# Kernel tuning notes

Hardware: AMD Instinct MI355X
Metric: run time of the kernel (lower is better)

The kernel has to match this reference:

```python
import jax, jax.numpy as jnp
from jax import lax
import numpy as np

B, S, D, COMP = 4, 1024, 512, 4


def setup_inputs() -> dict:
    key = jax.random.key(0)
    x = jax.random.normal(key, (B * S, D), dtype=jnp.float32)
    return {"x": x, "comp_rate": COMP, "seqlen": S}


def _merge_step(x, t, seq):
    # x: [seq, D], compacted so the k = seq - t valid tokens occupy rows 0..k-1.
    xn = jnp.roll(x, -1, axis=0)  # x[i+1] (wrap value never selected among valid pairs)
    # dist only feeds argmax (non-differentiable), mirror torch exactly; stop_gradient
    # keeps the vjp from saving residuals for this dead-for-gradients path.
    xg = lax.stop_gradient(x)
    dist = jnp.sum(xg * jnp.roll(xg, -1, axis=0), axis=-1)  # scalar_product metric
    j = jnp.arange(x.shape[0])
    dist = jnp.where(j < seq - 1 - t, dist, -jnp.inf)  # k-1 valid adjacent pairs
    mid = jnp.argmax(dist)
    jm = j[:, None]
    # rows < mid keep, row mid becomes (x[mid]+x[mid+1])/2, rows > mid shift left by 1
    return jnp.where(jm < mid, x, jnp.where(jm == mid, (x + xn) * 0.5, xn))


def _merge_sample(x, steps, seq):
    def body(carry, t):
        return _merge_step(carry, t, seq), None
    x, _ = lax.scan(body, x, jnp.arange(steps))
    return x


def reference(x, comp_rate, seqlen):
    d = x.shape[-1]
    b = x.shape[0] // seqlen
    n_comp = seqlen // comp_rate
    steps = seqlen - n_comp
    xb = x.reshape(b, seqlen, d)
    merged = jax.vmap(lambda xs: _merge_sample(xs, steps, seqlen))(xb)
    # torch smart_merge concatenates per-sample results along dim 0
    return merged[:, :n_comp].reshape(b * n_comp, d)
```

## Files before the change

### kernel.cpp

```cpp
#include <hip/hip_runtime.h>
#include <math.h>

#define S 1024
#define D 512
#define NCOMP (S / 4)
#define STEPS (S - NCOMP)
#define NEG_INF (-__builtin_inff())

__device__ int g_iter = 0;

__device__ __forceinline__ int   f2i(float x) { return __builtin_bit_cast(int, x); }
__device__ __forceinline__ float i2f(int x)   { return __builtin_bit_cast(float, x); }
__device__ __forceinline__ int   rfl(int x)   { return __builtin_amdgcn_readfirstlane(x); }

__device__ __forceinline__ unsigned fkey(float f) {
    unsigned u = __builtin_bit_cast(unsigned, f);
    return (u & 0x80000000u) ? ~u : (u | 0x80000000u);
}
__device__ __forceinline__ float unfkey(unsigned k) {
    unsigned u = (k & 0x80000000u) ? (k & 0x7fffffffu) : ~k;
    return __builtin_bit_cast(float, u);
}

__device__ __forceinline__ float wave_sum63(float x) {
    x += i2f(__builtin_amdgcn_update_dpp(0, f2i(x), 0x111, 0xF, 0xF, true));
    x += i2f(__builtin_amdgcn_update_dpp(0, f2i(x), 0x112, 0xF, 0xF, true));
    x += i2f(__builtin_amdgcn_update_dpp(0, f2i(x), 0x114, 0xF, 0xF, true));
    x += i2f(__builtin_amdgcn_update_dpp(0, f2i(x), 0x118, 0xF, 0xF, true));
    x += i2f(__builtin_amdgcn_update_dpp(0, f2i(x), 0x142, 0xA, 0xF, true));
    x += i2f(__builtin_amdgcn_update_dpp(0, f2i(x), 0x143, 0xC, 0xF, true));
    return x;
}

#define AMAX_STEP(ctrl, rm) do {                                                        \
    unsigned ok_ = (unsigned)__builtin_amdgcn_update_dpp((int)key, (int)key, (ctrl), (rm), 0xF, false); \
    int      oi_ = __builtin_amdgcn_update_dpp(bi, bi, (ctrl), (rm), 0xF, false);        \
    bool tk_ = (ok_ > key) || ((ok_ == key) && (oi_ < bi));                              \
    key = tk_ ? ok_ : key; bi = tk_ ? oi_ : bi;                                          \
} while (0)

struct Row { float4 a, b; };

__device__ __forceinline__ Row row_load(const float* vals, int slot, int lane) {
    const float4* p = (const float4*)(vals + (size_t)slot * D);
    Row r; r.a = p[lane * 2]; r.b = p[lane * 2 + 1]; return r;
}
__device__ __forceinline__ void row_store(float* vals, int slot, int lane, Row r) {
    float4* p = (float4*)(vals + (size_t)slot * D);
    p[lane * 2] = r.a; p[lane * 2 + 1] = r.b;
}
__device__ __forceinline__ Row row_avg(Row x, Row y) {
    Row r;
    r.a.x = (x.a.x + y.a.x) * 0.5f; r.a.y = (x.a.y + y.a.y) * 0.5f;
    r.a.z = (x.a.z + y.a.z) * 0.5f; r.a.w = (x.a.w + y.a.w) * 0.5f;
    r.b.x = (x.b.x + y.b.x) * 0.5f; r.b.y = (x.b.y + y.b.y) * 0.5f;
    r.b.z = (x.b.z + y.b.z) * 0.5f; r.b.w = (x.b.w + y.b.w) * 0.5f;
    return r;
}
__device__ __forceinline__ float dot8_partial(Row x, Row y) {
    float acc = x.a.x * y.a.x;
    acc += x.a.y * y.a.y; acc += x.a.z * y.a.z; acc += x.a.w * y.a.w;
    acc += x.b.x * y.b.x; acc += x.b.y * y.b.y; acc += x.b.z * y.b.z; acc += x.b.w * y.b.w;
    return acc;
}
__device__ __forceinline__ int lsr(int s) { return ((unsigned)s < (unsigned)S) ? s : 0; }
__device__ __forceinline__ int lsl(int s) { return ((unsigned)s <= (unsigned)S) ? s : 0; }

__device__ __forceinline__ void lds_argmax(const float* dist, int lane, float& v1, int& i1) {
    float av[16];
#pragma unroll
    for (int k = 0; k < 16; ++k) av[k] = dist[lane + 64 * k];
    float v8[8]; int k8[8];
#pragma unroll
    for (int k = 0; k < 8; ++k) { bool tk = av[k+8] > av[k]; v8[k] = tk ? av[k+8] : av[k]; k8[k] = tk ? (k+8) : k; }
    float v4[4]; int k4[4];
#pragma unroll
    for (int k = 0; k < 4; ++k) { bool tk = v8[k+4] > v8[k]; v4[k] = tk ? v8[k+4] : v8[k]; k4[k] = tk ? k8[k+4] : k8[k]; }
    float v2[2]; int k2[2];
#pragma unroll
    for (int k = 0; k < 2; ++k) { bool tk = v4[k+2] > v4[k]; v2[k] = tk ? v4[k+2] : v4[k]; k2[k] = tk ? k4[k+2] : k4[k]; }
    bool tk1 = v2[1] > v2[0];
    float lv = tk1 ? v2[1] : v2[0];
    int   lk = tk1 ? k2[1] : k2[0];
    unsigned key = fkey(lv);
    int bi = lane | (lk << 6);
    AMAX_STEP(0x111, 0xF); AMAX_STEP(0x112, 0xF);
    AMAX_STEP(0x114, 0xF); AMAX_STEP(0x118, 0xF);
    AMAX_STEP(0x142, 0xA); AMAX_STEP(0x143, 0xC);
    i1 = __builtin_amdgcn_readlane(bi, 63);
    v1 = unfkey((unsigned)__builtin_amdgcn_readlane((int)key, 63));
}

__device__ __attribute__((noinline)) void merge_A(float* __restrict__ vb,
                                                  const float* __restrict__ sd,
                                                  int* __restrict__ outIdx, int lane) {
    __shared__ int4 linksA[S + 1];
    __shared__ float distA[S];
    int4* links = linksA; float* dist = distA;

    for (int s = lane; s <= S; s += 64)
        links[s] = (s >= S) ? make_int4(S, S, S, 0)
                            : make_int4(s - 1, s + 1, (s + 2 <= S) ? (s + 2) : S, 0);
#pragma unroll
    for (int k = 0; k < 16; ++k) dist[lane + 64 * k] = sd[lane + 64 * k];

    float v1; int i1;
    lds_argmax(dist, lane, v1, i1);
    int m = i1;
    int4 L0 = links[m];
    int p = rfl(L0.x);
    int r = rfl(L0.y);
    int q = rfl(L0.z);
    bool hasp = (p >= 0), hasq = (q < S);
    int pp = hasp ? rfl(links[lsl(p)].x) : -1;
    int nq = hasq ? rfl(links[lsl(q)].y) : S;
    Row Rp  = row_load(vb, lsr(p),  lane);
    Row Rm  = row_load(vb, m,       lane);
    Row Rr  = row_load(vb, r,       lane);
    Row Rq  = row_load(vb, lsr(q),  lane);
    Row Rpp = row_load(vb, lsr(pp), lane);
    Row Rnq = row_load(vb, lsr(nq), lane);

#pragma unroll 1
    for (int t = 0; t < STEPS; ++t) {
        if (lane == 0) {
            links[m].y = q; links[m].z = nq;
            if (hasp) links[p].z = q;
            if (hasq) links[q].x = m;
            dist[m] = NEG_INF; dist[r] = NEG_INF;
            if (hasp) dist[p] = NEG_INF;
        }
        Row vm = row_avg(Rm, Rr);
        row_store(vb, m, lane, vm);
        if (t + 1 >= STEPS) break;

        float sp_ = wave_sum63(dot8_partial(Rp, vm));
        float sq_ = wave_sum63(dot8_partial(vm, Rq));
        float ndp = hasp ? i2f(__builtin_amdgcn_readlane(f2i(sp_), 63)) : NEG_INF;
        float ndm = hasq ? i2f(__builtin_amdgcn_readlane(f2i(sq_), 63)) : NEG_INF;

        lds_argmax(dist, lane, v1, i1);

        float best = v1; int bi = i1;
        if (hasp && (ndp > best || (ndp == best && p < bi))) { best = ndp; bi = p; }
        if (hasq && (ndm > best || (ndm == best && m < bi))) { best = ndm; bi = m; }
        const int m2 = bi;

        if (lane == 0) {
            if (hasp) dist[p] = ndp;
            if (hasq) dist[m] = ndm;
        }

        int4 Li = links[lsl(i1)];
        int p2 = rfl(Li.x);
        int r2 = rfl(Li.y);
        int q2 = rfl(Li.z);
        int4 Lp2 = links[lsl(p2)];
        int4 Lq2 = links[lsl(q2)];
        int pp2 = (p2 >= 0) ? rfl(Lp2.x) : -1;
        int nq2 = (q2 < S)  ? rfl(Lq2.y) : S;
        Row Sp  = (p2 == m)  ? vm : row_load(vb, lsr(p2),  lane);
        Row Si  = row_load(vb, lsr(i1), lane);
        Row Sr  = row_load(vb, lsr(r2), lane);
        Row Sq  = (q2 == m)  ? vm : row_load(vb, lsr(q2),  lane);
        Row Spp = (pp2 == m) ? vm : row_load(vb, lsr(pp2), lane);
        Row Snq = (nq2 == m) ? vm : row_load(vb, lsr(nq2), lane);

        if (m2 == m) {
            int nnq = S;
            if (nq < S) nnq = rfl(links[nq].y);
            Row Rnq2 = (nnq < S) ? row_load(vb, lsr(nnq), lane) : Rnq;
            Rm = vm; Rr = Rq; Rq = Rnq; Rnq = Rnq2;
            r = q; q = nq; nq = nnq;
            hasq = (q < S);
        } else if (m2 == p) {
            int npp = -1;
            if (pp >= 0) npp = rfl(links[pp].x);
            Row Rpp2 = (npp >= 0) ? row_load(vb, lsr(npp), lane) : Rpp;
            Rr = vm; Rm = Rp; Rp = Rpp; Rpp = Rpp2;
            r = m; m = p; p = pp; pp = npp;
            hasp = (p >= 0);
        } else {
            m = i1; p = p2; r = r2; q = q2; pp = pp2; nq = nq2;
            Rm = Si; Rr = Sr; Rp = Sp; Rq = Sq; Rpp = Spp; Rnq = Snq;
            hasp = (p >= 0); hasq = (q < S);
        }
    }

    if (lane == 0) {
        int s = 0;
        for (int i = 0; i < NCOMP; i += 2) {
            outIdx[i] = s;
            int4 Ls = links[s];
            if (i + 1 < NCOMP) outIdx[i + 1] = Ls.y;
            s = Ls.z;
        }
    }
}

__device__ __attribute__((noinline)) void merge_B(float* __restrict__ vb,
                                                  const float* __restrict__ sd,
                                                  int* __restrict__ outIdx, int lane) {
    __shared__ int4 linksB[S + 1];
    __shared__ float distB[S];
    int4* links = linksB; float* dist = distB;
    const int* li32 = (const int*)linksB;

    for (int s = lane; s <= S; s += 64)
        links[s] = (s >= S) ? make_int4(S, S, S, 0)
                            : make_int4(s - 1, s + 1, (s + 2 <= S) ? (s + 2) : S, 0);
#pragma unroll
    for (int k = 0; k < 16; ++k) dist[lane + 64 * k] = sd[lane + 64 * k];

    float v1; int i1;
    lds_argmax(dist, lane, v1, i1);
    int m = i1;
    int4 L0 = links[m];
    int p = rfl(L0.x);
    int r = rfl(L0.y);
    int q = rfl(L0.z);
    bool hasp = (p >= 0), hasq = (q < S);
    int pp = hasp ? rfl(links[lsl(p)].x) : -1;
    int nq = hasq ? rfl(links[lsl(q)].y) : S;
    Row Rp  = row_load(vb, lsr(p),  lane);
    Row Rm  = row_load(vb, m,       lane);
    Row Rr  = row_load(vb, r,       lane);
    Row Rq  = row_load(vb, lsr(q),  lane);
    bool pendP = false, pendQ = false;
    Row vmprev = Rm;

#pragma unroll 1
    for (int t = 0; t < STEPS; ++t) {
        Row RppL = row_load(vb, lsr(pp), lane);
        Row RnqL = row_load(vb, lsr(nq), lane);
        int wnnq = li32[lsl(nq) * 4 + 1];
        int wnpp = li32[lsl(pp) * 4 + 0];

        if (lane == 0) {
            links[m].y = q; links[m].z = nq;
            if (hasp) links[p].z = q;
            if (hasq) links[q].x = m;
            dist[m] = NEG_INF; dist[r] = NEG_INF;
            if (hasp) dist[p] = NEG_INF;
        }
        Row vm = row_avg(Rm, Rr);
        row_store(vb, m, lane, vm);
        if (t + 1 >= STEPS) break;

        float sp_ = wave_sum63(dot8_partial(Rp, vm));
        float sq_ = wave_sum63(dot8_partial(vm, Rq));
        float ndp = hasp ? i2f(__builtin_amdgcn_readlane(f2i(sp_), 63)) : NEG_INF;
        float ndm = hasq ? i2f(__builtin_amdgcn_readlane(f2i(sq_), 63)) : NEG_INF;

        lds_argmax(dist, lane, v1, i1);

        float best = v1; int bi = i1;
        if (hasp && (ndp > best || (ndp == best && p < bi))) { best = ndp; bi = p; }
        if (hasq && (ndm > best || (ndm == best && m < bi))) { best = ndm; bi = m; }
        const int m2 = bi;

        if (lane == 0) {
            if (hasp) dist[p] = ndp;
            if (hasq) dist[m] = ndm;
        }

        int4 Li = links[lsl(i1)];
        int p2 = rfl(Li.x);
        int r2 = rfl(Li.y);
        int q2 = rfl(Li.z);
        int pp2 = rfl(li32[lsl(p2) * 4 + 0]);
        int nq2 = rfl(li32[lsl(q2) * 4 + 1]);
        Row Si = row_load(vb, lsr(i1), lane);
        Row Sr = row_load(vb, lsr(r2), lane);
        Row Sp = (p2 == m) ? vm : row_load(vb, lsr(p2), lane);
        Row Sq = (q2 == m) ? vm : row_load(vb, lsr(q2), lane);

        Row Rpp_eff = pendP ? vmprev : RppL;
        Row Rnq_eff = pendQ ? vmprev : RnqL;

        if (m2 == m) {
            Rm = vm; Rr = Rq; Rq = Rnq_eff;
            r = q; q = nq; nq = rfl(wnnq);
            hasq = (q < S);
            pendP = false; pendQ = false;
        } else if (m2 == p) {
            Rr = vm; Rm = Rp; Rp = Rpp_eff;
            r = m; m = p; p = pp; pp = rfl(wnpp);
            hasp = (p >= 0);
            pendP = false; pendQ = false;
        } else {
            pendP = (pp2 == m); pendQ = (nq2 == m); vmprev = vm;
            m = i1; p = p2; r = r2; q = q2; pp = pp2; nq = nq2;
            Rm = Si; Rr = Sr; Rp = Sp; Rq = Sq;
            hasp = (p >= 0); hasq = (q < S);
        }
    }

    if (lane == 0) {
        int s = 0;
        for (int i = 0; i < NCOMP; i += 2) {
            outIdx[i] = s;
            int4 Ls = links[s];
            if (i + 1 < NCOMP) outIdx[i + 1] = Ls.y;
            s = Ls.z;
        }
    }
}

__global__ __launch_bounds__(256) void init_kernel(const float* __restrict__ x,
                                                   float* __restrict__ vals,
                                                   float* __restrict__ out) {
    const int blk = blockIdx.x, b = blk >> 4, g = blk & 15;
    const int tid = threadIdx.x, lane = tid & 63, w = tid >> 6;
    const float* xb = x + (size_t)b * S * D;
    if (blk == 0 && tid == 0) g_iter = g_iter + 1;
    if (vals != x) {
        float* vb = vals + (size_t)b * S * D;
        const float4* s4 = (const float4*)xb;
        float4* d4 = (float4*)vb;
        const int base = g * (S * D / 4 / 16);
        for (int i = tid; i < S * D / 4 / 16; i += 256) d4[base + i] = s4[base + i];
    }
    float* sd = out + (size_t)b * NCOMP * D;
#pragma unroll 1
    for (int j = 0; j < 16; ++j) {
        int pr = g * 64 + w * 16 + j;
        if (pr < S - 1) {
            Row A = row_load(xb, pr, lane);
            Row B = row_load(xb, pr + 1, lane);
            float t = wave_sum63(dot8_partial(A, B));
            if (lane == 63) sd[pr] = t;
        }
    }
    if (g == 0 && tid == 0) sd[S - 1] = NEG_INF;
}

__global__ __launch_bounds__(256, 1) void merge_kernel(float* __restrict__ vals,
                                                       float* __restrict__ out,
                                                       int nb) {
    const int blk = blockIdx.x, tid = threadIdx.x;
    const int b = blk, lane = tid & 63, wave = tid >> 6;
    float* vb = vals + (size_t)b * S * D;
    float* aux = out + (size_t)b * NCOMP * D;
    const float* sd = aux;
    int* outIdx = (int*)(aux + S);

    if (wave != 0) {
        float acc = 0.0f;
        for (int s = wave - 1; s < S; s += 3) {
            Row rr = row_load(vb, s, lane);
            acc += rr.a.x + rr.b.w;
        }
        if (acc == 1234.5678f) out[2050] = acc;
        return;
    }

    if (g_iter & 1) merge_A(vb, sd, outIdx, lane);
    else            merge_B(vb, sd, outIdx, lane);
}

__global__ __launch_bounds__(256) void gather_kernel(const float* __restrict__ vals,
                                                     float* __restrict__ out) {
    const int b = blockIdx.x, part = blockIdx.y;
    const float* vb = vals + (size_t)b * S * D;
    float* ob = out + (size_t)b * NCOMP * D;
    __shared__ int oi[NCOMP / 8];
    const int row0 = part * (NCOMP / 8);
    if (threadIdx.x < NCOMP / 8)
        oi[threadIdx.x] = ((const int*)(ob + S))[row0 + threadIdx.x];
    __syncthreads();
    const float4* v4 = (const float4*)vb;
    float4* o4 = (float4*)ob;
    const int per = (NCOMP / 8) * (D / 4);
    for (int idx = threadIdx.x; idx < per; idx += 256) {
        int row = idx >> 7, c = idx & 127;
        o4[(size_t)(row0 + row) * (D / 4) + c] = v4[(size_t)oi[row] * (D / 4) + c];
    }
}

extern "C" void kernel_launch(void* const* d_in, const int* in_sizes, int n_in,
                              void* d_out, int out_size, void* d_ws, size_t ws_size,
                              hipStream_t stream) {
    const float* x = (const float*)d_in[0];
    float* out = (float*)d_out;
    const int b = in_sizes[0] / (S * D);
    const size_t need = (size_t)in_sizes[0] * sizeof(float);
    float* vals = (ws_size >= need) ? (float*)d_ws : (float*)x;
    init_kernel<<<dim3(16 * b), dim3(256), 0, stream>>>(x, vals, out);
    merge_kernel<<<dim3(b), dim3(256), 0, stream>>>(vals, out, b);
    gather_kernel<<<dim3(b, 8), dim3(256), 0, stream>>>(vals, out);
}
```

Before: 1.041 ms.

## Offload per-step LDS argmax to a second wave via LDS mailbox handshake

Adds a merge_dual path in which wave 1 computes the argmax over the dist array while wave 0 does the row averaging, dot products and link updates for the same step. The two waves hand off through a small shared-memory mailbox using acquire/release atomics and spin-waits. Neighbour row and link loads are also issued earlier in the step. The aim is to take the argmax reduction off the serial critical path of each merge step. The cost is spin-wait overhead, and only calls with even g_iter use the new path, because the kernel still alternates it with the old single-wave version.

```diff
diff --git a/kernel.cpp b/kernel.cpp
--- a/kernel.cpp
+++ b/kernel.cpp
@@ -66,7 +66,8 @@
 __device__ __forceinline__ int lsr(int s) { return ((unsigned)s < (unsigned)S) ? s : 0; }
 __device__ __forceinline__ int lsl(int s) { return ((unsigned)s <= (unsigned)S) ? s : 0; }
 
-__device__ __forceinline__ void lds_argmax(const float* dist, int lane, float& v1, int& i1) {
+__device__ __forceinline__ void lds_argmax_raw(const float* dist, int lane,
+                                               unsigned& key_out, int& bi_out) {
     float av[16];
 #pragma unroll
     for (int k = 0; k < 16; ++k) av[k] = dist[lane + 64 * k];
@@ -87,120 +88,16 @@
     AMAX_STEP(0x111, 0xF); AMAX_STEP(0x112, 0xF);
     AMAX_STEP(0x114, 0xF); AMAX_STEP(0x118, 0xF);
     AMAX_STEP(0x142, 0xA); AMAX_STEP(0x143, 0xC);
-    i1 = __builtin_amdgcn_readlane(bi, 63);
-    v1 = unfkey((unsigned)__builtin_amdgcn_readlane((int)key, 63));
-}
-
-__device__ __attribute__((noinline)) void merge_A(float* __restrict__ vb,
-                                                  const float* __restrict__ sd,
-                                                  int* __restrict__ outIdx, int lane) {
-    __shared__ int4 linksA[S + 1];
-    __shared__ float distA[S];
-    int4* links = linksA; float* dist = distA;
-
-    for (int s = lane; s <= S; s += 64)
-        links[s] = (s >= S) ? make_int4(S, S, S, 0)
-                            : make_int4(s - 1, s + 1, (s + 2 <= S) ? (s + 2) : S, 0);
-#pragma unroll
-    for (int k = 0; k < 16; ++k) dist[lane + 64 * k] = sd[lane + 64 * k];
-
-    float v1; int i1;
-    lds_argmax(dist, lane, v1, i1);
-    int m = i1;
-    int4 L0 = links[m];
-    int p = rfl(L0.x);
-    int r = rfl(L0.y);
-    int q = rfl(L0.z);
-    bool hasp = (p >= 0), hasq = (q < S);
-    int pp = hasp ? rfl(links[lsl(p)].x) : -1;
-    int nq = hasq ? rfl(links[lsl(q)].y) : S;
-    Row Rp  = row_load(vb, lsr(p),  lane);
-    Row Rm  = row_load(vb, m,       lane);
-    Row Rr  = row_load(vb, r,       lane);
-    Row Rq  = row_load(vb, lsr(q),  lane);
-    Row Rpp = row_load(vb, lsr(pp), lane);
-    Row Rnq = row_load(vb, lsr(nq), lane);
-
-#pragma unroll 1
-    for (int t = 0; t < STEPS; ++t) {
-        if (lane == 0) {
-            links[m].y = q; links[m].z = nq;
-            if (hasp) links[p].z = q;
-            if (hasq) links[q].x = m;
-            dist[m] = NEG_INF; dist[r] = NEG_INF;
-            if (hasp) dist[p] = NEG_INF;
-        }
-        Row vm = row_avg(Rm, Rr);
-        row_store(vb, m, lane, vm);
-        if (t + 1 >= STEPS) break;
-
-        float sp_ = wave_sum63(dot8_partial(Rp, vm));
-        float sq_ = wave_sum63(dot8_partial(vm, Rq));
-        float ndp = hasp ? i2f(__builtin_amdgcn_readlane(f2i(sp_), 63)) : NEG_INF;
-        float ndm = hasq ? i2f(__builtin_amdgcn_readlane(f2i(sq_), 63)) : NEG_INF;
-
-        lds_argmax(dist, lane, v1, i1);
-
-        float best = v1; int bi = i1;
-        if (hasp && (ndp > best || (ndp == best && p < bi))) { best = ndp; bi = p; }
-        if (hasq && (ndm > best || (ndm == best && m < bi))) { best = ndm; bi = m; }
-        const int m2 = bi;
-
-        if (lane == 0) {
-            if (hasp) dist[p] = ndp;
-            if (hasq) dist[m] = ndm;
-        }
-
-        int4 Li = links[lsl(i1)];
-        int p2 = rfl(Li.x);
-        int r2 = rfl(Li.y);
-        int q2 = rfl(Li.z);
-        int4 Lp2 = links[lsl(p2)];
-        int4 Lq2 = links[lsl(q2)];
-        int pp2 = (p2 >= 0) ? rfl(Lp2.x) : -1;
-        int nq2 = (q2 < S)  ? rfl(Lq2.y) : S;
-        Row Sp  = (p2 == m)  ? vm : row_load(vb, lsr(p2),  lane);
-        Row Si  = row_load(vb, lsr(i1), lane);
-        Row Sr  = row_load(vb, lsr(r2), lane);
-        Row Sq  = (q2 == m)  ? vm : row_load(vb, lsr(q2),  lane);
-        Row Spp = (pp2 == m) ? vm : row_load(vb, lsr(pp2), lane);
-        Row Snq = (nq2 == m) ? vm : row_load(vb, lsr(nq2), lane);
-
-        if (m2 == m) {
-            int nnq = S;
-            if (nq < S) nnq = rfl(links[nq].y);
-            Row Rnq2 = (nnq < S) ? row_load(vb, lsr(nnq), lane) : Rnq;
-            Rm = vm; Rr = Rq; Rq = Rnq; Rnq = Rnq2;
-            r = q; q = nq; nq = nnq;
-            hasq = (q < S);
-        } else if (m2 == p) {
-            int npp = -1;
-            if (pp >= 0) npp = rfl(links[pp].x);
-            Row Rpp2 = (npp >= 0) ? row_load(vb, lsr(npp), lane) : Rpp;
-            Rr = vm; Rm = Rp; Rp = Rpp; Rpp = Rpp2;
-            r = m; m = p; p = pp; pp = npp;
-            hasp = (p >= 0);
-        } else {
-            m = i1; p = p2; r = r2; q = q2; pp = pp2; nq = nq2;
-            Rm = Si; Rr = Sr; Rp = Sp; Rq = Sq; Rpp = Spp; Rnq = Snq;
-            hasp = (p >= 0); hasq = (q < S);
-        }
-    }
-
-    if (lane == 0) {
-        int s = 0;
-        for (int i = 0; i < NCOMP; i += 2) {
-            outIdx[i] = s;
-            int4 Ls = links[s];
-            if (i + 1 < NCOMP) outIdx[i + 1] = Ls.y;
-            s = Ls.z;
-        }
-    }
-}
-
-__device__ __attribute__((noinline)) void merge_B(float* __restrict__ vb,
-                                                  const float* __restrict__ sd,
-                                                  int* __restrict__ outIdx, int lane) {
+    bi_out  = __builtin_amdgcn_readlane(bi, 63);
+    key_out = (unsigned)__builtin_amdgcn_readlane((int)key, 63);
+}
+__device__ __forceinline__ void lds_argmax(const float* dist, int lane, float& v1, int& i1) {
+    unsigned key; lds_argmax_raw(dist, lane, key, i1); v1 = unfkey(key);
+}
+
+__device__ __attribute__((noinline)) void merge_single(float* __restrict__ vb,
+                                                       const float* __restrict__ sd,
+                                                       int* __restrict__ outIdx, int lane) {
     __shared__ int4 linksB[S + 1];
     __shared__ float distB[S];
     int4* links = linksB; float* dist = distB;
@@ -307,6 +204,145 @@
     }
 }
 
+__device__ __attribute__((noinline)) void merge_dual(float* __restrict__ vb,
+                                                     const float* __restrict__ sd,
+                                                     int* __restrict__ outIdx,
+                                                     int lane, int wave,
+                                                     int* __restrict__ mbox) {
+    __shared__ int4 linksD[S + 1];
+    __shared__ float distD[S];
+    int4* links = linksD; float* dist = distD;
+    const int* li32 = (const int*)linksD;
+
+    if (wave == 1) {
+#pragma unroll 1
+        for (int t = 0; t < STEPS - 1; ++t) {
+            while (__hip_atomic_load(&mbox[0], __ATOMIC_ACQUIRE,
+                                     __HIP_MEMORY_SCOPE_WORKGROUP) < t + 1) {}
+            unsigned key; int bi;
+            lds_argmax_raw(dist, lane, key, bi);
+            if (lane == 0) {
+                mbox[2] = (int)key; mbox[3] = bi;
+                __hip_atomic_store(&mbox[1], t + 1, __ATOMIC_RELEASE,
+                                   __HIP_MEMORY_SCOPE_WORKGROUP);
+            }
+        }
+        return;
+    }
+
+    for (int s = lane; s <= S; s += 64)
+        links[s] = (s >= S) ? make_int4(S, S, S, 0)
+                            : make_int4(s - 1, s + 1, (s + 2 <= S) ? (s + 2) : S, 0);
+#pragma unroll
+    for (int k = 0; k < 16; ++k) dist[lane + 64 * k] = sd[lane + 64 * k];
+
+    float v1; int i1;
+    lds_argmax(dist, lane, v1, i1);
+    int m = i1;
+    int4 L0 = links[m];
+    int p = rfl(L0.x);
+    int r = rfl(L0.y);
+    int q = rfl(L0.z);
+    bool hasp = (p >= 0), hasq = (q < S);
+    int pp = hasp ? rfl(links[lsl(p)].x) : -1;
+    int nq = hasq ? rfl(links[lsl(q)].y) : S;
+    Row Rp  = row_load(vb, lsr(p),  lane);
+    Row Rm  = row_load(vb, m,       lane);
+    Row Rr  = row_load(vb, r,       lane);
+    Row Rq  = row_load(vb, lsr(q),  lane);
+    bool pendP = false, pendQ = false;
+    Row vmprev = Rm;
+
+#pragma unroll 1
+    for (int t = 0; t < STEPS - 1; ++t) {
+        Row RppL = row_load(vb, lsr(pp), lane);
+        Row RnqL = row_load(vb, lsr(nq), lane);
+        int wnnq = li32[lsl(nq) * 4 + 1];
+        int wnpp = li32[lsl(pp) * 4 + 0];
+
+        if (lane == 0) {
+            links[m].y = q; links[m].z = nq;
+            if (hasp) links[p].z = q;
+            if (hasq) links[q].x = m;
+            dist[m] = NEG_INF; dist[r] = NEG_INF;
+            if (hasp) dist[p] = NEG_INF;
+            __hip_atomic_store(&mbox[0], t + 1, __ATOMIC_RELEASE,
+                               __HIP_MEMORY_SCOPE_WORKGROUP);
+        }
+
+        Row vm = row_avg(Rm, Rr);
+        row_store(vb, m, lane, vm);
+        float sp_ = wave_sum63(dot8_partial(Rp, vm));
+        float sq_ = wave_sum63(dot8_partial(vm, Rq));
+        float ndp = hasp ? i2f(__builtin_amdgcn_readlane(f2i(sp_), 63)) : NEG_INF;
+        float ndm = hasq ? i2f(__builtin_amdgcn_readlane(f2i(sq_), 63)) : NEG_INF;
+
+        while (__hip_atomic_load(&mbox[1], __ATOMIC_ACQUIRE,
+                                 __HIP_MEMORY_SCOPE_WORKGROUP) < t + 1) {}
+        v1 = unfkey((unsigned)mbox[2]);
+        i1 = mbox[3];
+
+        float best = v1; int bi = i1;
+        if (hasp && (ndp > best || (ndp == best && p < bi))) { best = ndp; bi = p; }
+        if (hasq && (ndm > best || (ndm == best && m < bi))) { best = ndm; bi = m; }
+        const int m2 = bi;
+
+        if (lane == 0) {
+            if (hasp) dist[p] = ndp;
+            if (hasq) dist[m] = ndm;
+        }
+
+        int4 Li = links[lsl(i1)];
+        int p2 = rfl(Li.x);
+        int r2 = rfl(Li.y);
+        int q2 = rfl(Li.z);
+        int pp2 = rfl(li32[lsl(p2) * 4 + 0]);
+        int nq2 = rfl(li32[lsl(q2) * 4 + 1]);
+        Row Si = row_load(vb, lsr(i1), lane);
+        Row Sr = row_load(vb, lsr(r2), lane);
+        Row Sp = (p2 == m) ? vm : row_load(vb, lsr(p2), lane);
+        Row Sq = (q2 == m) ? vm : row_load(vb, lsr(q2), lane);
+
+        Row Rpp_eff = pendP ? vmprev : RppL;
+        Row Rnq_eff = pendQ ? vmprev : RnqL;
+
+        if (m2 == m) {
+            Rm = vm; Rr = Rq; Rq = Rnq_eff;
+            r = q; q = nq; nq = rfl(wnnq);
+            hasq = (q < S);
+            pendP = false; pendQ = false;
+        } else if (m2 == p) {
+            Rr = vm; Rm = Rp; Rp = Rpp_eff;
+            r = m; m = p; p = pp; pp = rfl(wnpp);
+            hasp = (p >= 0);
+            pendP = false; pendQ = false;
+        } else {
+            pendP = (pp2 == m); pendQ = (nq2 == m); vmprev = vm;
+            m = i1; p = p2; r = r2; q = q2; pp = pp2; nq = nq2;
+            Rm = Si; Rr = Sr; Rp = Sp; Rq = Sq;
+            hasp = (p >= 0); hasq = (q < S);
+        }
+    }
+
+    if (lane == 0) {
+        links[m].y = q; links[m].z = nq;
+        if (hasp) links[p].z = q;
+        if (hasq) links[q].x = m;
+    }
+    Row vm = row_avg(Rm, Rr);
+    row_store(vb, m, lane, vm);
+
+    if (lane == 0) {
+        int s = 0;
+        for (int i = 0; i < NCOMP; i += 2) {
+            outIdx[i] = s;
+            int4 Ls = links[s];
+            if (i + 1 < NCOMP) outIdx[i + 1] = Ls.y;
+            s = Ls.z;
+        }
+    }
+}
+
 __global__ __launch_bounds__(256) void init_kernel(const float* __restrict__ x,
                                                    float* __restrict__ vals,
                                                    float* __restrict__ out) {
@@ -338,25 +374,41 @@
 __global__ __launch_bounds__(256, 1) void merge_kernel(float* __restrict__ vals,
                                                        float* __restrict__ out,
                                                        int nb) {
+    __shared__ int mbox[4];
     const int blk = blockIdx.x, tid = threadIdx.x;
     const int b = blk, lane = tid & 63, wave = tid >> 6;
+    const int dual = !(g_iter & 1);
+    if (tid == 0) { mbox[0] = 0; mbox[1] = 0; }
+    __syncthreads();
+
     float* vb = vals + (size_t)b * S * D;
     float* aux = out + (size_t)b * NCOMP * D;
     const float* sd = aux;
     int* outIdx = (int*)(aux + S);
 
-    if (wave != 0) {
-        float acc = 0.0f;
-        for (int s = wave - 1; s < S; s += 3) {
-            Row rr = row_load(vb, s, lane);
-            acc += rr.a.x + rr.b.w;
-        }
-        if (acc == 1234.5678f) out[2050] = acc;
-        return;
-    }
-
-    if (g_iter & 1) merge_A(vb, sd, outIdx, lane);
-    else            merge_B(vb, sd, outIdx, lane);
+    if (dual) {
+        if (wave >= 2) {
+            float acc = 0.0f;
+            for (int s = wave - 2; s < S; s += 2) {
+                Row rr = row_load(vb, s, lane);
+                acc += rr.a.x + rr.b.w;
+            }
+            if (acc == 1234.5678f) out[2050] = acc;
+            return;
+        }
+        merge_dual(vb, sd, outIdx, lane, wave, mbox);
+    } else {
+        if (wave != 0) {
+            float acc = 0.0f;
+            for (int s = wave - 1; s < S; s += 3) {
+                Row rr = row_load(vb, s, lane);
+                acc += rr.a.x + rr.b.w;
+            }
+            if (acc == 1234.5678f) out[2050] = acc;
+            return;
+        }
+        merge_single(vb, sd, outIdx, lane);
+    }
 }
 
 __global__ __launch_bounds__(256) void gather_kernel(const float* __restrict__ vals,
```

New measurement: 998.6 us. -4.1%, faster.
